# Kernel tuning notes

Measured on AMD Instinct MI355X. Metric: run time of the kernel, lower is better.

## Reference

```python
import jax, jax.numpy as jnp
import numpy as np

N, D, P, T, M, H = 8192, 64, 32, 1, 50, 512
INTERVAL = 1.0
SIGMA = 1.0


def setup_inputs() -> dict:
    key = jax.random.key(0)
    k = jax.random.split(key, 9)
    in_dim = 1 + D + P  # [s, X, Y_t]
    return {
        "X0": jax.random.normal(k[0], (N, D), jnp.float32),
        "V0": jax.random.normal(k[1], (N,), jnp.float32),
        "Y": jax.random.normal(k[2], (N, T, P), jnp.float32),
        "theta": jax.random.normal(k[3], (D,), jnp.float32),
        "W1": jax.random.normal(k[4], (in_dim, H), jnp.float32) / np.sqrt(in_dim),
        "b1": jnp.zeros((H,), jnp.float32),
        "W2": jax.random.normal(k[5], (H, D), jnp.float32) / np.sqrt(H),
        "b2": jnp.zeros((D,), jnp.float32),
        "noise": jax.random.normal(k[6], (M, N, D), jnp.float32),
        "obs_index": 0,
    }


def reference(X0, V0, Y, theta, W1, b1, W2, b2, noise, obs_index):
    dt = jnp.float32(INTERVAL / M)
    sqrt_dt = jnp.sqrt(dt)
    Yt = Y[:, obs_index, :]  # (N, p) observation at this index

    def z_net(s, X):
        # Z_net(t, s, X, Y): MLP over [s, X, Y_t] -> (N, d)
        s_col = jnp.full((X.shape[0], 1), s, X.dtype)
        h = jnp.tanh(jnp.concatenate([s_col, X, Yt], axis=1) @ W1 + b1)
        return h @ W2 + b2

    def step(carry, xs):
        X, V = carry
        s, w = xs
        Wm = sqrt_dt * w  # Brownian increment
        Z = z_net(s, X)
        control = -jax.lax.stop_gradient(Z)  # -Z.detach()
        drift_V = 0.5 * jnp.sum(Z * Z, axis=1) + jnp.sum(control * Z, axis=1)
        V_new = V + dt * drift_V + jnp.sum(Z * Wm, axis=1)
        drift_X = (theta - X) + SIGMA * control  # b(theta, X) = theta - X (OU)
        X_new = X + dt * drift_X + SIGMA * Wm
        return (X_new, V_new), None

    times = jnp.arange(M, dtype=X0.dtype) * dt
    (X, V), _ = jax.lax.scan(step, (X0, V0), (times, noise))
    return X, V
```

## Files before the change

kernel.cpp:

```cpp
#include <hip/hip_runtime.h>
#include <hip/hip_bf16.h>

typedef __attribute__((ext_vector_type(4))) float f32x4;
typedef __attribute__((ext_vector_type(8))) short bf16x8;

#define NPART 8192
#define DDIM 64
#define PDIM 32
#define MSTEPS 50
#define HDIM 512
#define MB 16
#define A_LD 72
#define H_LD 520

__device__ __forceinline__ short f2bf(float f) {
  unsigned u = __builtin_bit_cast(unsigned, f);
  u = (u + 0x7fffu + ((u >> 16) & 1u)) >> 16;
  return (short)u;
}

__device__ __forceinline__ float fast_tanh(float xv) {
  float t = __expf(2.0f * xv);
  return 1.0f - 2.0f * __builtin_amdgcn_rcpf(t + 1.0f);
}

__device__ __forceinline__ unsigned pack_pair(float own) {
  int oi = __builtin_amdgcn_mov_dpp(__builtin_bit_cast(int, own),
                                    0xB1 , 0xF, 0xF, true);
  float other = __builtin_bit_cast(float, oi);
  unsigned out;
  asm("v_cvt_pk_bf16_f32 %0, %1, %2" : "=v"(out) : "v"(own), "v"(other));
  return out;
}

__global__ __launch_bounds__(512, 4) void sde_kernel(
    const float* __restrict__ X0, const float* __restrict__ V0,
    const float* __restrict__ Y, const float* __restrict__ theta,
    const float* __restrict__ W1, const float* __restrict__ b1,
    const float* __restrict__ W2, const float* __restrict__ b2,
    const float* __restrict__ noise, const int* __restrict__ obs_index,
    float* __restrict__ out) {
  __shared__ __align__(16) short lds_h[MB * H_LD];
  __shared__ __align__(16) short lds_a[MB * A_LD];
  __shared__ __align__(16) float lds_p[4 * 64 * 4];

  const int tid = threadIdx.x;
  const int w = tid >> 6;
  const int lane = tid & 63;
  const int c = lane & 15;
  const int g = lane >> 4;
  const int pb = blockIdx.x * MB;
  const int ntw = w & 3, kh = w >> 2;

  const float dt = 0.02f;
  const float sqdt = sqrtf(dt);

  {
    int m = tid >> 5, p = tid & 31;
    lds_p[tid] = Y[(size_t)(pb + m) * PDIM + (size_t)obs_index[0] * PDIM + p];
  }

  float x[4] = {0.f, 0.f, 0.f, 0.f};
  if (kh == 0) {
    #pragma unroll
    for (int r = 0; r < 4; ++r) {
      int m = 4 * g + r;
      x[r] = X0[(size_t)(pb + m) * DDIM + 16 * ntw + c];
      lds_a[m * A_LD + 16 * ntw + c] = f2bf(x[r]);
    }
  }
  __syncthreads();

  const int nj0 = 64 * w + c;
  f32x4 cy[4];
  float rv0[4];
  #pragma unroll
  for (int j = 0; j < 4; ++j) {
    rv0[j] = W1[nj0 + 16 * j];
    float bv = b1[nj0 + 16 * j];
    cy[j] = (f32x4){bv, bv, bv, bv};
  }
  for (int p = 0; p < PDIM; ++p) {
    float yv[4];
    #pragma unroll
    for (int r = 0; r < 4; ++r) yv[r] = lds_p[(4 * g + r) * PDIM + p];
    #pragma unroll
    for (int j = 0; j < 4; ++j) {
      float wv = W1[(size_t)(65 + p) * HDIM + nj0 + 16 * j];
      #pragma unroll
      for (int r = 0; r < 4; ++r) cy[j][r] = fmaf(yv[r], wv, cy[j][r]);
    }
  }

  bf16x8 bfr[4][2];
  #pragma unroll
  for (int j = 0; j < 4; ++j)
    #pragma unroll
    for (int kt = 0; kt < 2; ++kt)
      #pragma unroll
      for (int i = 0; i < 8; ++i)
        bfr[j][kt][i] =
            f2bf(W1[(size_t)(1 + 32 * kt + 8 * g + i) * HDIM + nj0 + 16 * j]);

  bf16x8 w2f[8];
  #pragma unroll
  for (int kt = 0; kt < 8; ++kt)
    #pragma unroll
    for (int i = 0; i < 8; ++i)
      w2f[kt][i] =
          f2bf(W2[(size_t)(256 * kh + 32 * kt + 8 * g + i) * DDIM + 16 * ntw + c]);

  const float thv = theta[16 * ntw + c];
  const float b2v = b2[16 * ntw + c];
  float vacc[4] = {0.f, 0.f, 0.f, 0.f};

  __syncthreads();

  for (int st = 0; st < MSTEPS; ++st) {
    const float s = st * dt;

    float wm[4];
    if (kh == 0) {
      const float* np_ =
          noise + ((size_t)st * NPART + pb + 4 * g) * DDIM + 16 * ntw + c;
      #pragma unroll
      for (int r = 0; r < 4; ++r) wm[r] = np_[(size_t)r * DDIM];
    }

    {
      const int abase = c * A_LD + 8 * g;
      bf16x8 af0 = *reinterpret_cast<const bf16x8*>(&lds_a[abase]);
      bf16x8 af1 = *reinterpret_cast<const bf16x8*>(&lds_a[abase + 32]);
      #pragma unroll
      for (int j = 0; j < 4; ++j) {
        f32x4 acc = cy[j];
        acc = __builtin_amdgcn_mfma_f32_16x16x32_bf16(af0, bfr[j][0], acc, 0, 0, 0);
        acc = __builtin_amdgcn_mfma_f32_16x16x32_bf16(af1, bfr[j][1], acc, 0, 0, 0);
        unsigned pk[4];
        #pragma unroll
        for (int r = 0; r < 4; ++r)
          pk[r] = pack_pair(fast_tanh(fmaf(s, rv0[j], acc[r])));
        if (!(lane & 1)) {
          #pragma unroll
          for (int r = 0; r < 4; ++r)
            *reinterpret_cast<unsigned*>(
                &lds_h[(4 * g + r) * H_LD + nj0 + 16 * j]) = pk[r];
        }
      }
    }

    __syncthreads();

    f32x4 acc2 = kh ? (f32x4){0.f, 0.f, 0.f, 0.f} : (f32x4){b2v, b2v, b2v, b2v};
    {
      const int hbase = c * H_LD + 256 * kh + 8 * g;
      #pragma unroll
      for (int kt = 0; kt < 8; ++kt)
        acc2 = __builtin_amdgcn_mfma_f32_16x16x32_bf16(
            *reinterpret_cast<const bf16x8*>(&lds_h[hbase + 32 * kt]), w2f[kt],
            acc2, 0, 0, 0);
    }
    float* pslot = &lds_p[(ntw * 64 + lane) * 4];
    if (kh) *reinterpret_cast<f32x4*>(pslot) = acc2;

    __syncthreads();

    if (!kh) {
      f32x4 part = *reinterpret_cast<const f32x4*>(pslot);
      unsigned apk[4];
      #pragma unroll
      for (int r = 0; r < 4; ++r) {
        float z = acc2[r] + part[r];
        float wmr = sqdt * wm[r];
        vacc[r] = fmaf(z, fmaf(-0.5f * dt, z, wmr), vacc[r]);
        x[r] = fmaf(dt, thv - x[r] - z, x[r]) + wmr;
        apk[r] = pack_pair(x[r]);
      }
      if (!(lane & 1)) {
        #pragma unroll
        for (int r = 0; r < 4; ++r)
          *reinterpret_cast<unsigned*>(
              &lds_a[(4 * g + r) * A_LD + 16 * ntw + c]) = apk[r];
      }
    }

    __syncthreads();
  }

  if (!kh) {
    #pragma unroll
    for (int r = 0; r < 4; ++r)
      out[(size_t)(pb + 4 * g + r) * DDIM + 16 * ntw + c] = x[r];
    #pragma unroll
    for (int mask = 1; mask <= 8; mask <<= 1)
      #pragma unroll
      for (int r = 0; r < 4; ++r) vacc[r] += __shfl_xor(vacc[r], mask);
    if (c == 0) {
      #pragma unroll
      for (int r = 0; r < 4; ++r)
        lds_p[(4 * g + r) * 4 + ntw] = vacc[r];
    }
  }
  __syncthreads();
  if (tid < MB)
    out[(size_t)NPART * DDIM + pb + tid] =
        V0[pb + tid] + lds_p[tid * 4] + lds_p[tid * 4 + 1] +
        lds_p[tid * 4 + 2] + lds_p[tid * 4 + 3];
}

extern "C" void kernel_launch(void* const* d_in, const int* in_sizes, int n_in,
                              void* d_out, int out_size, void* d_ws, size_t ws_size,
                              hipStream_t stream) {
  sde_kernel<<<512, 512, 0, stream>>>(
      (const float*)d_in[0], (const float*)d_in[1], (const float*)d_in[2],
      (const float*)d_in[3], (const float*)d_in[4], (const float*)d_in[5],
      (const float*)d_in[6], (const float*)d_in[7], (const float*)d_in[8],
      (const int*)d_in[9], (float*)d_out);
}
```

Baseline: 283.2 us.

## Switch MFMA to fp16, split X/V update across wave halves, dual accumulators

Switches operands and MFMA from bf16 to fp16, with round-toward-zero packing. Both wave halves now exchange their partial layer-2 sums through LDS. One half updates X and the other accumulates V, which splits the serial epilogue work between them. Layer-2 MFMAs use two independent accumulator chains to shorten the dependency chain. The tanh argument is folded into precomputed per-step constants, and noise loads use a running pointer. It also drops a redundant barrier. In exchange it doubles the LDS partial buffer and changes numerical rounding (fp16 range and precision).

Result: faster. 271.7 us (-4.1%).

```diff
diff --git a/kernel.cpp b/kernel.cpp
--- a/kernel.cpp
+++ b/kernel.cpp
@@ -1,8 +1,8 @@
 #include <hip/hip_runtime.h>
-#include <hip/hip_bf16.h>
+#include <hip/hip_fp16.h>
 
 typedef __attribute__((ext_vector_type(4))) float f32x4;
-typedef __attribute__((ext_vector_type(8))) short bf16x8;
+typedef __attribute__((ext_vector_type(8))) _Float16 f16x8;
 
 #define NPART 8192
 #define DDIM 64
@@ -13,23 +13,12 @@
 #define A_LD 72
 #define H_LD 520
 
-__device__ __forceinline__ short f2bf(float f) {
-  unsigned u = __builtin_bit_cast(unsigned, f);
-  u = (u + 0x7fffu + ((u >> 16) & 1u)) >> 16;
-  return (short)u;
-}
-
-__device__ __forceinline__ float fast_tanh(float xv) {
-  float t = __expf(2.0f * xv);
-  return 1.0f - 2.0f * __builtin_amdgcn_rcpf(t + 1.0f);
-}
-
 __device__ __forceinline__ unsigned pack_pair(float own) {
   int oi = __builtin_amdgcn_mov_dpp(__builtin_bit_cast(int, own),
                                     0xB1 , 0xF, 0xF, true);
   float other = __builtin_bit_cast(float, oi);
   unsigned out;
-  asm("v_cvt_pk_bf16_f32 %0, %1, %2" : "=v"(out) : "v"(own), "v"(other));
+  asm("v_cvt_pkrtz_f16_f32 %0, %1, %2" : "=v"(out) : "v"(own), "v"(other));
   return out;
 }
 
@@ -40,9 +29,9 @@
     const float* __restrict__ W2, const float* __restrict__ b2,
     const float* __restrict__ noise, const int* __restrict__ obs_index,
     float* __restrict__ out) {
-  __shared__ __align__(16) short lds_h[MB * H_LD];
-  __shared__ __align__(16) short lds_a[MB * A_LD];
-  __shared__ __align__(16) float lds_p[4 * 64 * 4];
+  __shared__ __align__(16) _Float16 lds_h[MB * H_LD];
+  __shared__ __align__(16) _Float16 lds_a[MB * A_LD];
+  __shared__ __align__(16) float lds_p[2048];
 
   const int tid = threadIdx.x;
   const int w = tid >> 6;
@@ -55,30 +44,28 @@
   const float dt = 0.02f;
   const float sqdt = sqrtf(dt);
 
-  {
-    int m = tid >> 5, p = tid & 31;
-    lds_p[tid] = Y[(size_t)(pb + m) * PDIM + (size_t)obs_index[0] * PDIM + p];
-  }
+  lds_p[tid] = Y[(size_t)(pb + (tid >> 5)) * PDIM + (size_t)obs_index[0] * PDIM +
+                 (tid & 31)];
 
   float x[4] = {0.f, 0.f, 0.f, 0.f};
-  if (kh == 0) {
+  if (kh) {
     #pragma unroll
     for (int r = 0; r < 4; ++r) {
       int m = 4 * g + r;
       x[r] = X0[(size_t)(pb + m) * DDIM + 16 * ntw + c];
-      lds_a[m * A_LD + 16 * ntw + c] = f2bf(x[r]);
+      lds_a[m * A_LD + 16 * ntw + c] = (_Float16)x[r];
     }
   }
   __syncthreads();
 
   const int nj0 = 64 * w + c;
-  f32x4 cy[4];
-  float rv0[4];
+  f32x4 cy2[4];
+  float rv02[4];
   #pragma unroll
   for (int j = 0; j < 4; ++j) {
-    rv0[j] = W1[nj0 + 16 * j];
+    rv02[j] = 2.0f * W1[nj0 + 16 * j];
     float bv = b1[nj0 + 16 * j];
-    cy[j] = (f32x4){bv, bv, bv, bv};
+    cy2[j] = (f32x4){bv, bv, bv, bv};
   }
   for (int p = 0; p < PDIM; ++p) {
     float yv[4];
@@ -88,11 +75,15 @@
     for (int j = 0; j < 4; ++j) {
       float wv = W1[(size_t)(65 + p) * HDIM + nj0 + 16 * j];
       #pragma unroll
-      for (int r = 0; r < 4; ++r) cy[j][r] = fmaf(yv[r], wv, cy[j][r]);
-    }
-  }
-
-  bf16x8 bfr[4][2];
+      for (int r = 0; r < 4; ++r) cy2[j][r] = fmaf(yv[r], wv, cy2[j][r]);
+    }
+  }
+  #pragma unroll
+  for (int j = 0; j < 4; ++j)
+    #pragma unroll
+    for (int r = 0; r < 4; ++r) cy2[j][r] *= 2.0f;
+
+  f16x8 bfr[4][2];
   #pragma unroll
   for (int j = 0; j < 4; ++j)
     #pragma unroll
@@ -100,46 +91,52 @@
       #pragma unroll
       for (int i = 0; i < 8; ++i)
         bfr[j][kt][i] =
-            f2bf(W1[(size_t)(1 + 32 * kt + 8 * g + i) * HDIM + nj0 + 16 * j]);
-
-  bf16x8 w2f[8];
+            (_Float16)W1[(size_t)(1 + 32 * kt + 8 * g + i) * HDIM + nj0 + 16 * j];
+
+  f16x8 w2f[8];
   #pragma unroll
   for (int kt = 0; kt < 8; ++kt)
     #pragma unroll
     for (int i = 0; i < 8; ++i)
       w2f[kt][i] =
-          f2bf(W2[(size_t)(256 * kh + 32 * kt + 8 * g + i) * DDIM + 16 * ntw + c]);
+          (_Float16)W2[(size_t)(256 * kh + 32 * kt + 8 * g + i) * DDIM + 16 * ntw + c];
 
   const float thv = theta[16 * ntw + c];
   const float b2v = b2[16 * ntw + c];
   float vacc[4] = {0.f, 0.f, 0.f, 0.f};
 
-  __syncthreads();
+  const float* np_ = noise + ((size_t)pb + 4 * g) * DDIM + 16 * ntw + c;
 
   for (int st = 0; st < MSTEPS; ++st) {
     const float s = st * dt;
 
     float wm[4];
-    if (kh == 0) {
-      const float* np_ =
-          noise + ((size_t)st * NPART + pb + 4 * g) * DDIM + 16 * ntw + c;
-      #pragma unroll
-      for (int r = 0; r < 4; ++r) wm[r] = np_[(size_t)r * DDIM];
-    }
+    #pragma unroll
+    for (int r = 0; r < 4; ++r) wm[r] = np_[(size_t)r * DDIM];
+    np_ += (size_t)NPART * DDIM;
+
+    float csr[4][4];
+    #pragma unroll
+    for (int j = 0; j < 4; ++j)
+      #pragma unroll
+      for (int r = 0; r < 4; ++r) csr[j][r] = fmaf(s, rv02[j], cy2[j][r]);
 
     {
       const int abase = c * A_LD + 8 * g;
-      bf16x8 af0 = *reinterpret_cast<const bf16x8*>(&lds_a[abase]);
-      bf16x8 af1 = *reinterpret_cast<const bf16x8*>(&lds_a[abase + 32]);
+      f16x8 af0 = *reinterpret_cast<const f16x8*>(&lds_a[abase]);
+      f16x8 af1 = *reinterpret_cast<const f16x8*>(&lds_a[abase + 32]);
       #pragma unroll
       for (int j = 0; j < 4; ++j) {
-        f32x4 acc = cy[j];
-        acc = __builtin_amdgcn_mfma_f32_16x16x32_bf16(af0, bfr[j][0], acc, 0, 0, 0);
-        acc = __builtin_amdgcn_mfma_f32_16x16x32_bf16(af1, bfr[j][1], acc, 0, 0, 0);
+        f32x4 acc = (f32x4){0.f, 0.f, 0.f, 0.f};
+        acc = __builtin_amdgcn_mfma_f32_16x16x32_f16(af0, bfr[j][0], acc, 0, 0, 0);
+        acc = __builtin_amdgcn_mfma_f32_16x16x32_f16(af1, bfr[j][1], acc, 0, 0, 0);
         unsigned pk[4];
         #pragma unroll
-        for (int r = 0; r < 4; ++r)
-          pk[r] = pack_pair(fast_tanh(fmaf(s, rv0[j], acc[r])));
+        for (int r = 0; r < 4; ++r) {
+          float e = __expf(fmaf(2.0f, acc[r], csr[j][r]));
+          float th = fmaf(-2.0f, __builtin_amdgcn_rcpf(e + 1.0f), 1.0f);
+          pk[r] = pack_pair(th);
+        }
         if (!(lane & 1)) {
           #pragma unroll
           for (int r = 0; r < 4; ++r)
@@ -151,46 +148,64 @@
 
     __syncthreads();
 
-    f32x4 acc2 = kh ? (f32x4){0.f, 0.f, 0.f, 0.f} : (f32x4){b2v, b2v, b2v, b2v};
+    f32x4 a2a = kh ? (f32x4){0.f, 0.f, 0.f, 0.f} : (f32x4){b2v, b2v, b2v, b2v};
+    f32x4 a2b = (f32x4){0.f, 0.f, 0.f, 0.f};
     {
       const int hbase = c * H_LD + 256 * kh + 8 * g;
       #pragma unroll
-      for (int kt = 0; kt < 8; ++kt)
-        acc2 = __builtin_amdgcn_mfma_f32_16x16x32_bf16(
-            *reinterpret_cast<const bf16x8*>(&lds_h[hbase + 32 * kt]), w2f[kt],
-            acc2, 0, 0, 0);
-    }
-    float* pslot = &lds_p[(ntw * 64 + lane) * 4];
-    if (kh) *reinterpret_cast<f32x4*>(pslot) = acc2;
+      for (int kt = 0; kt < 4; ++kt) {
+        a2a = __builtin_amdgcn_mfma_f32_16x16x32_f16(
+            *reinterpret_cast<const f16x8*>(&lds_h[hbase + 64 * kt]), w2f[2 * kt],
+            a2a, 0, 0, 0);
+        a2b = __builtin_amdgcn_mfma_f32_16x16x32_f16(
+            *reinterpret_cast<const f16x8*>(&lds_h[hbase + 64 * kt + 32]),
+            w2f[2 * kt + 1], a2b, 0, 0, 0);
+      }
+    }
+    f32x4 acc2;
+    #pragma unroll
+    for (int r = 0; r < 4; ++r) acc2[r] = a2a[r] + a2b[r];
+
+    *reinterpret_cast<f32x4*>(&lds_p[(kh * 256 + ntw * 64 + lane) * 4]) = acc2;
 
     __syncthreads();
 
-    if (!kh) {
-      f32x4 part = *reinterpret_cast<const f32x4*>(pslot);
-      unsigned apk[4];
-      #pragma unroll
-      for (int r = 0; r < 4; ++r) {
-        float z = acc2[r] + part[r];
-        float wmr = sqdt * wm[r];
-        vacc[r] = fmaf(z, fmaf(-0.5f * dt, z, wmr), vacc[r]);
-        x[r] = fmaf(dt, thv - x[r] - z, x[r]) + wmr;
-        apk[r] = pack_pair(x[r]);
+    {
+      f32x4 oth = *reinterpret_cast<const f32x4*>(
+          &lds_p[((1 - kh) * 256 + ntw * 64 + lane) * 4]);
+      if (kh) {
+        unsigned apk[4];
+        #pragma unroll
+        for (int r = 0; r < 4; ++r) {
+          float z = acc2[r] + oth[r];
+          float wmr = sqdt * wm[r];
+          x[r] = fmaf(dt, thv - x[r] - z, x[r]) + wmr;
+          apk[r] = pack_pair(x[r]);
+        }
+        if (!(lane & 1)) {
+          #pragma unroll
+          for (int r = 0; r < 4; ++r)
+            *reinterpret_cast<unsigned*>(
+                &lds_a[(4 * g + r) * A_LD + 16 * ntw + c]) = apk[r];
+        }
+      } else {
+        #pragma unroll
+        for (int r = 0; r < 4; ++r) {
+          float z = acc2[r] + oth[r];
+          float wmr = sqdt * wm[r];
+          vacc[r] = fmaf(z, fmaf(-0.5f * dt, z, wmr), vacc[r]);
+        }
       }
-      if (!(lane & 1)) {
-        #pragma unroll
-        for (int r = 0; r < 4; ++r)
-          *reinterpret_cast<unsigned*>(
-              &lds_a[(4 * g + r) * A_LD + 16 * ntw + c]) = apk[r];
-      }
     }
 
     __syncthreads();
   }
 
-  if (!kh) {
+  if (kh) {
     #pragma unroll
     for (int r = 0; r < 4; ++r)
       out[(size_t)(pb + 4 * g + r) * DDIM + 16 * ntw + c] = x[r];
+  } else {
     #pragma unroll
     for (int mask = 1; mask <= 8; mask <<= 1)
       #pragma unroll
```
